# Performance work log

Hardware: AMD Instinct MI355X
Metric: run time of the kernel (lower is better)

The kernel has to match this reference:

```python
import jax, jax.numpy as jnp
import numpy as np

NEG_SLOPE = 0.01  # F.leaky_relu default used in the original forward


def setup_inputs() -> dict:
    key = jax.random.key(0)
    ks = jax.random.split(key, 6)
    B, N, D = 2, 4096, 128
    s = 1.0 / np.sqrt(D)
    return {
        "embed_feat": jax.random.normal(ks[0], (B, N, D), jnp.float32),
        "predict_G": 1,
        "W_demand": jax.random.normal(ks[1], (D,), jnp.float32) * s,
        "b_demand": jnp.zeros((1,), jnp.float32),
        "Wa": jax.random.normal(ks[2], (D, D), jnp.float32) * s,
        "w_l": jax.random.normal(ks[3], (D,), jnp.float32) * s,
        "w_r": jax.random.normal(ks[4], (D,), jnp.float32) * s,
    }


def reference(embed_feat, predict_G, W_demand, b_demand, Wa, w_l, w_r):
    # demands: sigmoid(Linear(D->1)) -> [B, N]
    demands = jax.nn.sigmoid(embed_feat @ W_demand + b_demand[0])
    if not predict_G:
        return (demands, None)
    # proj = Wa(x): [B, N, D]  (torch Linear: x @ Wa.T)
    proj = jnp.einsum('bnd,ed->bne', embed_feat, Wa)
    # per-node scalar scores; A[b,i,j] = l[b,i] + r[b,j] (vectorized form of the O(N^2) loop)
    l = proj @ w_l  # [B, N]
    r = proj @ w_r  # [B, N]
    A = jax.nn.leaky_relu(l[:, :, None] + r[:, None, :], negative_slope=NEG_SLOPE)
    # original softmax over dim=1 of [N, N, 1] == over j axis
    Q = jax.nn.softmax(A, axis=2)  # [B, N, N]
    # rel_Ds[b,i,j] = demands[b,i]
    Gs = Q * demands[:, :, None]
    return (demands, Gs)
```

## Files before the change

kernel.cpp:

```cpp
#include <hip/hip_runtime.h>
#include <stdint.h>

#define N 4096
#define B 2
#define D 128
#define LOG2E 1.4426950408889634f

__device__ __forceinline__ float lrelu(float t) { return t > 0.f ? t : 0.01f * t; }

__global__ __launch_bounds__(256) void k1_uvec(
    const float* __restrict__ Wa,
    const float* __restrict__ w_l,
    const float* __restrict__ w_r,
    float* __restrict__ u) {
    __shared__ float2 pl[4][64];
    __shared__ float2 pr[4][64];
    int t = threadIdx.x;
    int d2 = t & 63;
    int h = t >> 6;
    const float2* Wa2 = (const float2*)Wa;
    float2 al = make_float2(0.f, 0.f), ar = make_float2(0.f, 0.f);
    #pragma unroll 8
    for (int k = 0; k < 32; ++k) {
        int e = h * 32 + k;
        float2 w = Wa2[e * 64 + d2];
        float wl = w_l[e];
        float wr = w_r[e];
        al.x += w.x * wl; al.y += w.y * wl;
        ar.x += w.x * wr; ar.y += w.y * wr;
    }
    pl[h][d2] = al; pr[h][d2] = ar;
    __syncthreads();
    if (t < 64) {
        float2 s = make_float2(0.f, 0.f);
        #pragma unroll
        for (int hh = 0; hh < 4; ++hh) { s.x += pl[hh][t].x; s.y += pl[hh][t].y; }
        ((float2*)u)[t] = s;
    } else if (t < 128) {
        int dd = t - 64;
        float2 s = make_float2(0.f, 0.f);
        #pragma unroll
        for (int hh = 0; hh < 4; ++hh) { s.x += pr[hh][dd].x; s.y += pr[hh][dd].y; }
        ((float2*)(u + D))[dd] = s;
    }
}

__global__ __launch_bounds__(256) void k2_rows(
    const float* __restrict__ x,
    const float* __restrict__ Wd,
    const float* __restrict__ bd,
    const float* __restrict__ u,
    float* __restrict__ out_dem,
    float* __restrict__ lv,
    float* __restrict__ rv) {
    int lane = threadIdx.x & 63;
    int row = blockIdx.x * 4 + (threadIdx.x >> 6);
    float2 xv = ((const float2*)(x + (size_t)row * D))[lane];
    float2 ul2 = ((const float2*)u)[lane];
    float2 ur2 = ((const float2*)(u + D))[lane];
    float2 wv = ((const float2*)Wd)[lane];
    float pl = xv.x * ul2.x + xv.y * ul2.y;
    float pr = xv.x * ur2.x + xv.y * ur2.y;
    float pd = xv.x * wv.x + xv.y * wv.y;
    #pragma unroll
    for (int m = 32; m >= 1; m >>= 1) {
        pl += __shfl_xor(pl, m, 64);
        pr += __shfl_xor(pr, m, 64);
        pd += __shfl_xor(pd, m, 64);
    }
    if (lane == 0) {
        float dem = 1.f / (1.f + __expf(-(pd + bd[0])));
        out_dem[row] = dem;
        lv[row] = pl * LOG2E;
        rv[row] = pr * LOG2E;
    }
}

__global__ __launch_bounds__(256) void k3_main(
    const float* __restrict__ lv, const float* __restrict__ rv,
    const float* __restrict__ dem_f,
    float* __restrict__ out_g) {
    __shared__ float sr[N];
    __shared__ float redmax[4];
    __shared__ float redsum[4][4];
    int tid = threadIdx.x;
    int b = blockIdx.x >> 10;
    int i0 = (blockIdx.x & 1023) << 2;
    const float* rb = rv + b * N;
    float lmax = -3.402823466e38f;
    #pragma unroll
    for (int k = 0; k < N / 256; ++k) {
        float v = rb[tid + k * 256];
        sr[tid + k * 256] = v;
        lmax = fmaxf(lmax, v);
    }
    #pragma unroll
    for (int m = 32; m >= 1; m >>= 1) lmax = fmaxf(lmax, __shfl_xor(lmax, m, 64));
    if ((tid & 63) == 0) redmax[tid >> 6] = lmax;
    __syncthreads();
    float rmax = fmaxf(fmaxf(redmax[0], redmax[1]), fmaxf(redmax[2], redmax[3]));

    int rowbase = b * N + i0;
    float lr_[4], mr[4], s[4];
    #pragma unroll
    for (int q = 0; q < 4; ++q) {
        lr_[q] = lv[rowbase + q];
        mr[q] = lrelu(lr_[q] + rmax);
        s[q] = 0.f;
    }
    #pragma unroll 2
    for (int k = 0; k < N / 256; ++k) {
        float r = sr[tid + k * 256];
        #pragma unroll
        for (int q = 0; q < 4; ++q) s[q] += exp2f(lrelu(lr_[q] + r) - mr[q]);
    }
    #pragma unroll
    for (int m = 32; m >= 1; m >>= 1) {
        #pragma unroll
        for (int q = 0; q < 4; ++q) s[q] += __shfl_xor(s[q], m, 64);
    }
    if ((tid & 63) == 0) {
        #pragma unroll
        for (int q = 0; q < 4; ++q) redsum[tid >> 6][q] = s[q];
    }
    __syncthreads();
    float sc[4];
    #pragma unroll
    for (int q = 0; q < 4; ++q) {
        float den = redsum[0][q] + redsum[1][q] + redsum[2][q] + redsum[3][q];
        sc[q] = dem_f[rowbase + q] / den;
    }
    const float4* rb4 = (const float4*)rb;
    size_t gbase = (size_t)b * N * N + (size_t)i0 * N;
    #pragma unroll
    for (int it = 0; it < 4; ++it) {
        int idx = it * 256 + tid;
        float4 r4 = rb4[idx];
        #pragma unroll
        for (int q = 0; q < 4; ++q) {
            float4 o;
            o.x = exp2f(lrelu(lr_[q] + r4.x) - mr[q]) * sc[q];
            o.y = exp2f(lrelu(lr_[q] + r4.y) - mr[q]) * sc[q];
            o.z = exp2f(lrelu(lr_[q] + r4.z) - mr[q]) * sc[q];
            o.w = exp2f(lrelu(lr_[q] + r4.w) - mr[q]) * sc[q];
            *(float4*)(out_g + gbase + (size_t)q * N + (size_t)idx * 4) = o;
        }
    }
}

extern "C" void kernel_launch(void* const* d_in, const int* in_sizes, int n_in,
                              void* d_out, int out_size, void* d_ws, size_t ws_size,
                              hipStream_t stream) {
    const float* x  = (const float*)d_in[0];
    const float* Wd = (const float*)d_in[2];
    const float* bd = (const float*)d_in[3];
    const float* Wa = (const float*)d_in[4];
    const float* wl = (const float*)d_in[5];
    const float* wr = (const float*)d_in[6];

    float* ws = (float*)d_ws;
    float* u  = ws;
    float* lv = ws + 256;
    float* rv = ws + 256 + 8192;

    float* out     = (float*)d_out;
    float* out_dem = out;
    float* out_g   = out + B * N;

    hipLaunchKernelGGL(k1_uvec, dim3(1), dim3(256), 0, stream, Wa, wl, wr, u);
    hipLaunchKernelGGL(k2_rows, dim3(B * N / 4), dim3(256), 0, stream,
                       x, Wd, bd, u, out_dem, lv, rv);
    hipLaunchKernelGGL(k3_main, dim3(B * N / 4), dim3(256), 0, stream,
                       lv, rv, out_dem, out_g);
}
```

Measured before the change: 156.9 us.

## Process 8 rows per block, vectorize r loads, reuse LDS, nontemporal stores

The main kernel now handles 8 output rows per block instead of 4, which halves the number of blocks and the redundant per-block loading and max-reduction of the r vector. The r vector is staged into shared memory with float4 loads, and the output phase reads it back from LDS instead of global memory. Output stores use nontemporal builtins so the 128 MB write stream bypasses the caches. The cost is more registers per thread and fewer blocks to spread across CUs.

Measured after the change: 163.2 us. +4.1%, slower.

```diff
diff --git a/kernel.cpp b/kernel.cpp
--- a/kernel.cpp
+++ b/kernel.cpp
@@ -4,7 +4,10 @@
 #define N 4096
 #define B 2
 #define D 128
+#define ROWS 8
 #define LOG2E 1.4426950408889634f
+
+using f32x4 = __attribute__((ext_vector_type(4))) float;
 
 __device__ __forceinline__ float lrelu(float t) { return t > 0.f ? t : 0.01f * t; }
 
@@ -80,19 +83,21 @@
     const float* __restrict__ lv, const float* __restrict__ rv,
     const float* __restrict__ dem_f,
     float* __restrict__ out_g) {
-    __shared__ float sr[N];
+    __shared__ float4 sr4[N / 4];
     __shared__ float redmax[4];
-    __shared__ float redsum[4][4];
+    __shared__ float redsum[4][ROWS];
     int tid = threadIdx.x;
-    int b = blockIdx.x >> 10;
-    int i0 = (blockIdx.x & 1023) << 2;
+    int b = blockIdx.x / (N / ROWS);
+    int i0 = (blockIdx.x % (N / ROWS)) * ROWS;
     const float* rb = rv + b * N;
+    const float4* rb4 = (const float4*)rb;
+
     float lmax = -3.402823466e38f;
     #pragma unroll
-    for (int k = 0; k < N / 256; ++k) {
-        float v = rb[tid + k * 256];
-        sr[tid + k * 256] = v;
-        lmax = fmaxf(lmax, v);
+    for (int k = 0; k < N / 4 / 256; ++k) {
+        float4 v = rb4[tid + k * 256];
+        sr4[tid + k * 256] = v;
+        lmax = fmaxf(lmax, fmaxf(fmaxf(v.x, v.y), fmaxf(v.z, v.w)));
     }
     #pragma unroll
     for (int m = 32; m >= 1; m >>= 1) lmax = fmaxf(lmax, __shfl_xor(lmax, m, 64));
@@ -101,49 +106,49 @@
     float rmax = fmaxf(fmaxf(redmax[0], redmax[1]), fmaxf(redmax[2], redmax[3]));
 
     int rowbase = b * N + i0;
-    float lr_[4], mr[4], s[4];
+    float lr_[ROWS], mr[ROWS], s[ROWS];
     #pragma unroll
-    for (int q = 0; q < 4; ++q) {
+    for (int q = 0; q < ROWS; ++q) {
         lr_[q] = lv[rowbase + q];
         mr[q] = lrelu(lr_[q] + rmax);
         s[q] = 0.f;
     }
+    const float* sr = (const float*)sr4;
     #pragma unroll 2
     for (int k = 0; k < N / 256; ++k) {
         float r = sr[tid + k * 256];
         #pragma unroll
-        for (int q = 0; q < 4; ++q) s[q] += exp2f(lrelu(lr_[q] + r) - mr[q]);
+        for (int q = 0; q < ROWS; ++q) s[q] += exp2f(lrelu(lr_[q] + r) - mr[q]);
     }
     #pragma unroll
     for (int m = 32; m >= 1; m >>= 1) {
         #pragma unroll
-        for (int q = 0; q < 4; ++q) s[q] += __shfl_xor(s[q], m, 64);
+        for (int q = 0; q < ROWS; ++q) s[q] += __shfl_xor(s[q], m, 64);
     }
     if ((tid & 63) == 0) {
         #pragma unroll
-        for (int q = 0; q < 4; ++q) redsum[tid >> 6][q] = s[q];
+        for (int q = 0; q < ROWS; ++q) redsum[tid >> 6][q] = s[q];
     }
     __syncthreads();
-    float sc[4];
+    float sc[ROWS];
     #pragma unroll
-    for (int q = 0; q < 4; ++q) {
+    for (int q = 0; q < ROWS; ++q) {
         float den = redsum[0][q] + redsum[1][q] + redsum[2][q] + redsum[3][q];
         sc[q] = dem_f[rowbase + q] / den;
     }
-    const float4* rb4 = (const float4*)rb;
     size_t gbase = (size_t)b * N * N + (size_t)i0 * N;
     #pragma unroll
     for (int it = 0; it < 4; ++it) {
         int idx = it * 256 + tid;
-        float4 r4 = rb4[idx];
+        float4 r4 = sr4[idx];
         #pragma unroll
-        for (int q = 0; q < 4; ++q) {
-            float4 o;
+        for (int q = 0; q < ROWS; ++q) {
+            f32x4 o;
             o.x = exp2f(lrelu(lr_[q] + r4.x) - mr[q]) * sc[q];
             o.y = exp2f(lrelu(lr_[q] + r4.y) - mr[q]) * sc[q];
             o.z = exp2f(lrelu(lr_[q] + r4.z) - mr[q]) * sc[q];
             o.w = exp2f(lrelu(lr_[q] + r4.w) - mr[q]) * sc[q];
-            *(float4*)(out_g + gbase + (size_t)q * N + (size_t)idx * 4) = o;
+            __builtin_nontemporal_store(o, (f32x4*)(out_g + gbase + (size_t)q * N + (size_t)idx * 4));
         }
     }
 }
@@ -170,6 +175,6 @@
     hipLaunchKernelGGL(k1_uvec, dim3(1), dim3(256), 0, stream, Wa, wl, wr, u);
     hipLaunchKernelGGL(k2_rows, dim3(B * N / 4), dim3(256), 0, stream,
                        x, Wd, bd, u, out_dem, lv, rv);
-    hipLaunchKernelGGL(k3_main, dim3(B * N / 4), dim3(256), 0, stream,
+    hipLaunchKernelGGL(k3_main, dim3(B * N / ROWS), dim3(256), 0, stream,
                        lv, rv, out_dem, out_g);
 }
```
